# Kernel optimization log

Measured on AMD Instinct MI355X. Metric: run time of the kernel, lower is better.

The kernel has to match this reference:

```python
import jax, jax.numpy as jnp
import numpy as np

B, T, D, H = 2, 1024, 1024, 16
K = D            # key_dim = hidden * expand_k (1.0)
V = 2 * D        # value_dim = hidden * expand_v (2.0)
DK, DV = K // H, V // H
I = 2816         # SwiGLU intermediate
CONV = 4
EPS = 1e-6


def rmsnorm(x, w, eps=EPS):
    return x * jax.lax.rsqrt(jnp.mean(x * x, -1, keepdims=True) + eps) * w


def l2norm(x, eps=EPS):
    return x * jax.lax.rsqrt(jnp.sum(x * x, -1, keepdims=True) + eps)


def short_conv(x, w):
    # depthwise causal conv1d (kernel CONV, no bias) + silu; x [B,T,C], w [C,CONV]
    kern = w.T[:, None, :]  # [CONV, 1, C]
    y = jax.lax.conv_general_dilated(
        x, kern, (1,), [(CONV - 1, 0)],
        dimension_numbers=('NWC', 'WIO', 'NWC'),
        feature_group_count=x.shape[-1])
    return jax.nn.silu(y)


def setup_inputs() -> dict:
    key = jax.random.key(0)
    ks = jax.random.split(key, 20)
    p = lambda i, shape, s=0.02: jax.random.normal(ks[i], shape, jnp.float32) * s
    return dict(
        x=jax.random.normal(ks[0], (B, T, D), jnp.float32),
        norm1_w=jnp.ones((D,), jnp.float32),
        wq=p(1, (D, K)), wk=p(2, (D, K)), wv=p(3, (D, V)),
        conv_q=p(4, (K, CONV), 0.3), conv_k=p(5, (K, CONV), 0.3), conv_v=p(6, (V, CONV), 0.3),
        wb=p(7, (D, H)), wa=p(8, (D, H)),
        A_log=jnp.log(jax.random.uniform(ks[9], (H,), jnp.float32, 1.0, 16.0)),
        dt_bias=jnp.log(jnp.expm1(jax.random.uniform(ks[10], (H,), jnp.float32, 0.001, 0.1))),
        wg=p(11, (D, V)),
        o_norm_w=jnp.ones((DV,), jnp.float32),
        wo=p(12, (V, D)),
        norm2_w=jnp.ones((D,), jnp.float32),
        w1=p(13, (D, I)), w2=p(14, (I, D)), w3=p(15, (D, I)),
    )


def reference(x, norm1_w, wq, wk, wv, conv_q, conv_k, conv_v, wb, wa,
              A_log, dt_bias, wg, o_norm_w, wo, norm2_w, w1, w2, w3):
    h = rmsnorm(x, norm1_w)
    # projections + short causal conv (silu)
    q = short_conv(h @ wq, conv_q).reshape(B, T, H, DK)
    k = short_conv(h @ wk, conv_k).reshape(B, T, H, DK)
    v = short_conv(h @ wv, conv_v).reshape(B, T, H, DV)
    q = l2norm(q) * (DK ** -0.5)
    k = l2norm(k)
    beta = jax.nn.sigmoid(h @ wb)                              # [B,T,H]
    # mamba-style decay gate: g = -exp(A_log) * softplus(a + dt_bias)
    g = -jnp.exp(A_log) * jax.nn.softplus(h @ wa + dt_bias)   # [B,T,H]

    # gated delta rule: S_t = exp(g_t)*S_{t-1}; u_t = beta_t*(v_t - k_t^T S_t);
    # S_t += k_t u_t^T; o_t = q_t^T S_t
    def step(S, inp):
        qt, kt, vt, gt, bt = inp                               # [B,H,*]
        S = S * jnp.exp(gt)[..., None, None]
        u = (vt - jnp.einsum('bhk,bhkv->bhv', kt, S)) * bt[..., None]
        S = S + kt[..., None] * u[:, :, None, :]
        ot = jnp.einsum('bhk,bhkv->bhv', qt, S)
        return S, ot

    S0 = jnp.zeros((B, H, DK, DV), x.dtype)
    seq = (q.transpose(1, 0, 2, 3), k.transpose(1, 0, 2, 3),
           v.transpose(1, 0, 2, 3), g.transpose(1, 0, 2), beta.transpose(1, 0, 2))
    _, o = jax.lax.scan(step, S0, seq)
    o = o.transpose(1, 0, 2, 3)                                # [B,T,H,DV]

    # output gate: per-head RMSNorm * swish(gate), then out-projection
    gate = (h @ wg).reshape(B, T, H, DV)
    o = rmsnorm(o, o_norm_w) * gate * jax.nn.sigmoid(gate)
    x = x + o.reshape(B, T, V) @ wo

    # SwiGLU MLP with residual
    h2 = rmsnorm(x, norm2_w)
    return x + (jax.nn.silu(h2 @ w1) * (h2 @ w3)) @ w2
```

## Files before the change

### kernel.cpp

```cpp
#include <hip/hip_runtime.h>
#include <stdint.h>

typedef unsigned short u16;
typedef float f32x4 __attribute__((ext_vector_type(4)));
typedef __bf16 bf16x8 __attribute__((ext_vector_type(8)));
typedef unsigned short u16x8 __attribute__((ext_vector_type(8)));

#define N1P 6272

__device__ __forceinline__ u16 f2bf(float f) {
    union { float f; uint32_t u; } v; v.f = f;
    uint32_t u = v.u;
    return (u16)((u + 0x7FFFu + ((u >> 16) & 1u)) >> 16);
}
__device__ __forceinline__ float bf2f(u16 h) {
    union { uint32_t u; float f; } v; v.u = ((uint32_t)h) << 16; return v.f;
}
__device__ __forceinline__ float sigm(float x) { return 1.f / (1.f + __expf(-x)); }

__device__ __forceinline__ void async16(const u16* g, u16* l) {
    __builtin_amdgcn_global_load_lds((const __attribute__((address_space(1))) void*)g,
                                     (__attribute__((address_space(3))) void*)l, 16, 0, 0);
}

__device__ __forceinline__ int swz64(int row, int col) {
    return row * 128 + ((((col >> 3) ^ (row & 7)) << 3) + (col & 7)) * 2;
}
__device__ __forceinline__ bf16x8 frag64(const u16* m, int rowbase, int lane, int kk) {
    const int row = rowbase + (lane & 15);
    const int unit = (lane >> 4) + (kk << 2);
    return *(const bf16x8*)((const char*)m + row * 128 + ((unit ^ (row & 7)) << 4));
}

struct TJob { const float* src; u16* dst; int rows, cols, rowOff, rowStride, nOut, blkBase, gx, mode; };
struct TJobs { TJob j[10]; };

__global__ __launch_bounds__(256) void k_transpose_all(TJobs jobs, int njobs) {
    __shared__ float tile[32][33];
    const int bid = blockIdx.x;
    int ji = 0;
#pragma unroll
    for (int i = 1; i < 10; ++i)
        if (i < njobs && bid >= jobs.j[i].blkBase) ji = i;
    const TJob J = jobs.j[ji];
    const int bx = bid - J.blkBase;
    const int n0 = (bx % J.gx) * 32, k0 = (bx / J.gx) * 32;
    const int tx = threadIdx.x, ty = threadIdx.y;
#pragma unroll
    for (int j = 0; j < 32; j += 8) {
        int r = k0 + ty + j, c = n0 + tx;
        tile[ty + j][tx] = (r < J.rows && c < J.cols) ? J.src[(size_t)r * J.cols + c] : 0.f;
    }
    __syncthreads();
#pragma unroll
    for (int j = 0; j < 32; j += 8) {
        int n = n0 + ty + j, k = k0 + tx;
        if (n < J.nOut) {
            int drow = (J.mode == 0) ? (J.rowOff + n * J.rowStride)
                                     : (J.rowOff + ((n >> 4) << 5) + (n & 15));
            J.dst[(size_t)drow * J.rows + k] = f2bf(tile[tx][ty + j]);
        }
    }
}

__global__ __launch_bounds__(256) void k_rmsnorm(const float* __restrict__ x, const float* __restrict__ w,
                                                 u16* __restrict__ out) {
    const int row = blockIdx.x, tid = threadIdx.x, lane = tid & 63, wave = tid >> 6;
    const float4 v = ((const float4*)(x + (size_t)row * 1024))[tid];
    float ss = v.x * v.x + v.y * v.y + v.z * v.z + v.w * v.w;
#pragma unroll
    for (int o = 1; o < 64; o <<= 1) ss += __shfl_xor(ss, o);
    __shared__ float sred[4];
    if (lane == 0) sred[wave] = ss;
    __syncthreads();
    const float tot = sred[0] + sred[1] + sred[2] + sred[3];
    const float rn = rsqrtf(tot * (1.f / 1024.f) + 1e-6f);
    const float4 wv = ((const float4*)w)[tid];
    uint2 pk;
    pk.x = (uint32_t)f2bf(v.x * rn * wv.x) | ((uint32_t)f2bf(v.y * rn * wv.y) << 16);
    pk.y = (uint32_t)f2bf(v.z * rn * wv.z) | ((uint32_t)f2bf(v.w * rn * wv.w) << 16);
    *(uint2*)&out[(size_t)row * 1024 + tid * 4] = pk;
}

template <int TILE, int EPI>
__global__ __launch_bounds__(512) void k_gemm(const u16* __restrict__ A, const u16* __restrict__ Bt,
                                              void* __restrict__ Cout, const float* __restrict__ Res,
                                              int N, int Kd) {
    __shared__ __align__(16) char smem[TILE * 512];
    u16* Asb = (u16*)smem;
    u16* Bsb = (u16*)(smem + TILE * 256);
    constexpr int MB = 2048 / TILE;
    const int q = (int)gridDim.x >> 3;
    const int bid = blockIdx.x;
    const int wg = (bid & 7) * q + (bid >> 3);
    const int bm = wg & (MB - 1), bn = wg / MB;
    const int tid = threadIdx.x, lane = tid & 63, wave = tid >> 6;
    const int wm = wave >> 2, wn = wave & 3;
    constexpr int RS = TILE / 2, CS = TILE / 4;
    constexpr int FRM = RS / 16, FRN = CS / 16;
    constexpr int IS = TILE / 64;

    const int srow = wave * 8 + (lane >> 3);
    const int scol = ((lane & 7) ^ (lane >> 3)) * 8;
    const u16* gA = A + (size_t)(bm * TILE + srow) * Kd + scol;
    const u16* gB = Bt + (size_t)(bn * TILE + srow) * Kd + scol;

    f32x4 acc[FRM][FRN] = {};
    const int NT = Kd >> 6;

#pragma unroll
    for (int j = 0; j < IS; ++j) {
        async16(gA + (size_t)j * 64 * Kd, Asb + j * 4096 + wave * 512);
        async16(gB + (size_t)j * 64 * Kd, Bsb + j * 4096 + wave * 512);
    }
    asm volatile("s_waitcnt vmcnt(0)" ::: "memory");
    __syncthreads();

    int buf = 0;
    for (int t = 0; t < NT; ++t) {
        if (t + 1 < NT) {
            const int k0 = (t + 1) << 6;
            const int bo = (buf ^ 1) * TILE * 64;
#pragma unroll
            for (int j = 0; j < IS; ++j) {
                async16(gA + (size_t)j * 64 * Kd + k0, Asb + bo + j * 4096 + wave * 512);
                async16(gB + (size_t)j * 64 * Kd + k0, Bsb + bo + j * 4096 + wave * 512);
            }
        }
        const u16* Ab = Asb + buf * TILE * 64;
        const u16* Bb = Bsb + buf * TILE * 64;
#pragma unroll
        for (int kk = 0; kk < 2; ++kk) {
            bf16x8 af[FRM], bfr[FRN];
#pragma unroll
            for (int mi = 0; mi < FRM; ++mi) af[mi] = frag64(Ab, wm * RS + mi * 16, lane, kk);
#pragma unroll
            for (int ni = 0; ni < FRN; ++ni) bfr[ni] = frag64(Bb, wn * CS + ni * 16, lane, kk);
#pragma unroll
            for (int mi = 0; mi < FRM; ++mi)
#pragma unroll
                for (int ni = 0; ni < FRN; ++ni)
                    acc[mi][ni] = __builtin_amdgcn_mfma_f32_16x16x32_bf16(af[mi], bfr[ni], acc[mi][ni], 0, 0, 0);
        }
        asm volatile("s_waitcnt vmcnt(0)" ::: "memory");
        __syncthreads();
        buf ^= 1;
    }

    const int rsub = (lane >> 4) * 4;
    const int csub = lane & 15;

    if constexpr (EPI == 1) {
        float* ctile = (float*)smem;
#pragma unroll
        for (int mi = 0; mi < FRM; ++mi)
#pragma unroll
            for (int ni = 0; ni < FRN; ++ni)
#pragma unroll
                for (int r = 0; r < 4; ++r)
                    ctile[(wm * 32 + mi * 16 + rsub + r) * 68 + wn * 16 + ni * 16 + csub] = acc[mi][ni][r];
        __syncthreads();
#pragma unroll
        for (int k = 0; k < 2; ++k) {
            const int f = (tid + k * 512) * 4;
            const int r = f >> 6, c = f & 63;
            float4 v = *(const float4*)&ctile[r * 68 + c];
            const float4 rv = *(const float4*)&Res[(size_t)(bm * 64 + r) * N + bn * 64 + c];
            v.x += rv.x; v.y += rv.y; v.z += rv.z; v.w += rv.w;
            *(float4*)&((float*)Cout)[(size_t)(bm * 64 + r) * N + bn * 64 + c] = v;
        }
    } else if constexpr (EPI == 2) {
        u16* ctile = (u16*)smem;
#pragma unroll
        for (int mi = 0; mi < FRM; ++mi)
#pragma unroll
            for (int ni = 0; ni < FRN; ++ni)
#pragma unroll
                for (int r = 0; r < 4; ++r)
                    ctile[(wm * 64 + mi * 16 + rsub + r) * 132 + wn * 32 + ni * 16 + csub] =
                        f2bf(acc[mi][ni][r]);
        __syncthreads();
#pragma unroll
        for (int k = 0; k < 4; ++k) {
            const int f = (tid + k * 512) * 8;
            const int r = f >> 7, c = f & 127;
            *(u16x8*)&((u16*)Cout)[(size_t)(bm * 128 + r) * N + bn * 128 + c] =
                *(const u16x8*)&ctile[r * 132 + c];
        }
    } else {
        u16* ctile = (u16*)smem;
#pragma unroll
        for (int mi = 0; mi < FRM; ++mi)
#pragma unroll
            for (int r = 0; r < 4; ++r) {
                const float u1 = acc[mi][0][r];
                const float u3 = acc[mi][1][r];
                ctile[(wm * 64 + mi * 16 + rsub + r) * 68 + wn * 16 + csub] =
                    f2bf(u1 * sigm(u1) * u3);
            }
        __syncthreads();
#pragma unroll
        for (int k = 0; k < 2; ++k) {
            const int f = (tid + k * 512) * 8;
            const int r = f >> 6, c = f & 63;
            *(u16x8*)&((u16*)Cout)[(size_t)(bm * 128 + r) * N + bn * 64 + c] =
                *(const u16x8*)&ctile[r * 68 + c];
        }
    }
}

__global__ __launch_bounds__(256) void k_conv(const u16* __restrict__ P, const float* __restrict__ cwq,
                                              const float* __restrict__ cwk, const float* __restrict__ cwv,
                                              const float* __restrict__ A_log, const float* __restrict__ dtb,
                                              u16* __restrict__ Qb, u16* __restrict__ Kb,
                                              u16* __restrict__ Vb, float* __restrict__ Gl,
                                              float* __restrict__ Bbuf) {
    const int bid = blockIdx.x;
    const int row = (bid & 7) * 256 + (bid >> 3);
    const int t = row & 1023;
    const int tid = threadIdx.x;
    const long prow = (long)row * N1P;
#pragma unroll
    for (int p = 0; p < 2; ++p) {
        const int g = p * 256 + tid;
        const int c = g * 8;
        u16x8 taps[4];
#pragma unroll
        for (int j = 0; j < 4; ++j) {
            const int tt = t - 3 + j;
            if (tt >= 0) taps[j] = *(const u16x8*)&P[prow + (long)(j - 3) * N1P + c];
            else         taps[j] = u16x8{};
        }
        const float* cw = (c < 1024) ? (cwq + c * 4)
                          : (c < 2048) ? (cwk + (c - 1024) * 4)
                                       : (cwv + (c - 2048) * 4);
        float y[8];
#pragma unroll
        for (int e = 0; e < 8; ++e) {
            const float4 w = ((const float4*)cw)[e];
            float v = bf2f(taps[0][e]) * w.x + bf2f(taps[1][e]) * w.y +
                      bf2f(taps[2][e]) * w.z + bf2f(taps[3][e]) * w.w;
            y[e] = v * sigm(v);
        }
        if (c < 2048) {
            float ss = 0.f;
#pragma unroll
            for (int e = 0; e < 8; ++e) ss += y[e] * y[e];
            ss += __shfl_xor(ss, 1); ss += __shfl_xor(ss, 2); ss += __shfl_xor(ss, 4);
            const float rn = rsqrtf(ss + 1e-6f);
            const float sc = (c < 1024) ? rn * 0.125f : rn;
            u16x8 o;
#pragma unroll
            for (int e = 0; e < 8; ++e) o[e] = f2bf(y[e] * sc);
            if (c < 1024) *(u16x8*)&Qb[(size_t)row * 1024 + c] = o;
            else          *(u16x8*)&Kb[(size_t)row * 1024 + (c - 1024)] = o;
        } else {
            u16x8 o;
#pragma unroll
            for (int e = 0; e < 8; ++e) o[e] = f2bf(y[e]);
            *(u16x8*)&Vb[(size_t)row * 2048 + (c - 2048)] = o;
        }
    }
    if (tid < 32) {
        const int h = tid & 15;
        const float val = bf2f(P[prow + 4096 + tid]);
        if (tid < 16) {
            Bbuf[(size_t)row * 16 + h] = sigm(val);
        } else {
            const float a = val + dtb[h];
            const float sp = (a > 15.f) ? a : log1pf(__expf(a));
            Gl[(size_t)row * 16 + h] = -__expf(A_log[h]) * sp;
        }
    }
}

__global__ __launch_bounds__(256) void k_scan1(
    const u16* __restrict__ Qb, const u16* __restrict__ Kb, const u16* __restrict__ Vb,
    const float* __restrict__ Gl, const float* __restrict__ Bb,
    u16* __restrict__ CHW, u16* __restrict__ CHM, u16* __restrict__ CHQc,
    u16* __restrict__ CHKcT, u16* __restrict__ CHU0T, float* __restrict__ CHcC) {
    __shared__ __align__(16) char sm[66048];
    u16* Ql   = (u16*)(sm);
    u16* Kl   = (u16*)(sm + 8192);
    u16* VTb  = (u16*)(sm + 16384);
    u16* KT1b = (u16*)(sm + 32768);
    u16* Mim  = (u16*)(sm + 40960);
    u16* MTim = (u16*)(sm + 49152);
    u16* Tb   = (u16*)(sm + 57344);
    float* Tl    = (float*)sm;
    float* gcs   = (float*)(sm + 65536);
    float* betal = (float*)(sm + 65792);

    const int blk = blockIdx.x;
    const int bb = blk >> 8, h = (blk >> 4) & 15, ch = blk & 15;
    const int bhc = blk;
    const int tid = threadIdx.x, lane = tid & 63, wave = tid >> 6;
    const long rowbase = (long)bb * 1024 + ch * 64;

    if (tid < 64) {
        gcs[tid] = Gl[(rowbase + tid) * 16 + h];
        betal[tid] = Bb[(rowbase + tid) * 16 + h];
    }
    for (int u = tid; u < 512; u += 256) {
        int r = u >> 3, c8 = u & 7;
        uint4 kv = *(const uint4*)&Kb[(rowbase + r) * 1024 + h * 64 + c8 * 8];
        uint4 qv = *(const uint4*)&Qb[(rowbase + r) * 1024 + h * 64 + c8 * 8];
        int b = r * 128 + ((c8 ^ (r & 7)) << 4);
        *(uint4*)((char*)Kl + b) = kv;
        *(uint4*)((char*)Ql + b) = qv;
    }
    __syncthreads();
    if (wave == 0) {
        float g = gcs[lane];
#pragma unroll
        for (int off = 1; off < 64; off <<= 1) {
            float n = __shfl_up(g, off, 64);
            if (lane >= off) g += n;
        }
        gcs[lane] = g;
    }
    for (int u = tid; u < 1024; u += 256) {
        int r = u >> 4, c8 = u & 15;
        u16x8 vv = *(const u16x8*)&Vb[(rowbase + r) * 2048 + h * 128 + c8 * 8];
        float bsc = betal[r];
#pragma unroll
        for (int j = 0; j < 8; ++j) {
            int dv = c8 * 8 + j;
            *(u16*)((char*)VTb + swz64(dv, r)) = f2bf(bf2f(vv[j]) * bsc);
        }
    }
    f32x4 aQK[4] = {}, aKK[4] = {};
#pragma unroll
    for (int nt = 0; nt < 4; ++nt)
#pragma unroll
        for (int kk = 0; kk < 2; ++kk) {
            bf16x8 bq = frag64(Kl, nt * 16, lane, kk);
            aQK[nt] = __builtin_amdgcn_mfma_f32_16x16x32_bf16(frag64(Ql, wave * 16, lane, kk), bq, aQK[nt], 0, 0, 0);
            aKK[nt] = __builtin_amdgcn_mfma_f32_16x16x32_bf16(frag64(Kl, wave * 16, lane, kk), bq, aKK[nt], 0, 0, 0);
        }
    __syncthreads();

    const float gcsC = gcs[63];
    float am[4][4];
#pragma unroll
    for (int nt = 0; nt < 4; ++nt)
#pragma unroll
        for (int reg = 0; reg < 4; ++reg) {
            int t = wave * 16 + ((lane >> 4) << 2) + reg;
            int i = nt * 16 + (lane & 15);
            float dec = __expf(gcs[t] - gcs[i]);
            float mv = (i <= t) ? dec * aQK[nt][reg] : 0.f;
            *(u16*)((char*)CHM + (size_t)bhc * 8192 + swz64(t, i)) = f2bf(mv);
            float a = (i < t) ? betal[t] * dec * aKK[nt][reg] : 0.f;
            am[nt][reg] = -a;
            u16 amb = f2bf(-a);
            *(u16*)((char*)Mim + swz64(t, i)) = amb;
            *(u16*)((char*)MTim + swz64(i, t)) = amb;
        }
    for (int e = tid; e < 4096; e += 256) {
        int r = e >> 6, c = e & 63;
        int ib = swz64(r, c);
        float qv = bf2f(*(const u16*)((const char*)Ql + ib)) * __expf(gcs[r]);
        *(u16*)((char*)CHQc + (size_t)bhc * 8192 + ib) = f2bf(qv);
        float kv = bf2f(*(const u16*)((const char*)Kl + ib));
        int ob = swz64(c, r);
        *(u16*)((char*)KT1b + ob) = f2bf(kv * betal[r] * __expf(gcs[r]));
        *(u16*)((char*)CHKcT + (size_t)bhc * 8192 + ob) = f2bf(kv * __expf(gcsC - gcs[r]));
    }
    if (tid == 0) CHcC[bhc] = __expf(gcsC);
    __syncthreads();

#pragma unroll
    for (int nt = 0; nt < 4; ++nt)
#pragma unroll
        for (int reg = 0; reg < 4; ++reg) {
            int t = wave * 16 + ((lane >> 4) << 2) + reg;
            int i = nt * 16 + (lane & 15);
            float tv = (t == i) ? 1.f : am[nt][reg];
            Tl[t * 64 + i] = tv;
            *(u16*)((char*)Tb + swz64(t, i)) = f2bf(tv);
        }
    __syncthreads();

    const int hi = wave * 16 + 15;
#pragma unroll
    for (int j = 1; j <= 5; ++j) {
        f32x4 aM[4] = {};
#pragma unroll
        for (int nt = 0; nt < 4; ++nt) {
            if (nt * 16 > hi - (1 << j)) continue;
#pragma unroll
            for (int kk = 0; kk < 2; ++kk) {
                if (kk * 32 > hi) break;
                aM[nt] = __builtin_amdgcn_mfma_f32_16x16x32_bf16(
                    frag64(Mim, wave * 16, lane, kk), frag64(MTim, nt * 16, lane, kk), aM[nt], 0, 0, 0);
            }
        }
        __syncthreads();
#pragma unroll
        for (int nt = 0; nt < 4; ++nt)
#pragma unroll
            for (int reg = 0; reg < 4; ++reg) {
                int t = wave * 16 + ((lane >> 4) << 2) + reg;
                int i = nt * 16 + (lane & 15);
                float mv = (t - i >= (1 << j)) ? aM[nt][reg] : 0.f;
                u16 mb = f2bf(mv);
                *(u16*)((char*)Mim + swz64(t, i)) = mb;
                *(u16*)((char*)MTim + swz64(i, t)) = mb;
            }
        __syncthreads();
        f32x4 aT[4];
#pragma unroll
        for (int nt = 0; nt < 4; ++nt)
#pragma unroll
            for (int reg = 0; reg < 4; ++reg) {
                int t = wave * 16 + ((lane >> 4) << 2) + reg;
                int i = nt * 16 + (lane & 15);
                aT[nt][reg] = Tl[t * 64 + i];
            }
#pragma unroll
        for (int nt = 0; nt < 4; ++nt) {
            if (nt * 16 > hi - (1 << j)) continue;
#pragma unroll
            for (int kk = 0; kk < 2; ++kk) {
                if (kk * 32 > hi) break;
                aT[nt] = __builtin_amdgcn_mfma_f32_16x16x32_bf16(
                    frag64(Tb, wave * 16, lane, kk), frag64(MTim, nt * 16, lane, kk), aT[nt], 0, 0, 0);
            }
        }
#pragma unroll
        for (int nt = 0; nt < 4; ++nt)
#pragma unroll
            for (int reg = 0; reg < 4; ++reg) {
                int t = wave * 16 + ((lane >> 4) << 2) + reg;
                int i = nt * 16 + (lane & 15);
                Tl[t * 64 + i] = aT[nt][reg];
                *(u16*)((char*)Tb + swz64(t, i)) = f2bf(aT[nt][reg]);
            }
    }
    __syncthreads();

    {
        f32x4 aW[4] = {};
#pragma unroll
        for (int nt = 0; nt < 4; ++nt)
#pragma unroll
            for (int kk = 0; kk < 2; ++kk) {
                if (kk * 32 > hi) break;
                aW[nt] = __builtin_amdgcn_mfma_f32_16x16x32_bf16(
                    frag64(Tb, wave * 16, lane, kk), frag64(KT1b, nt * 16, lane, kk), aW[nt], 0, 0, 0);
            }
#pragma unroll
        for (int nt = 0; nt < 4; ++nt)
#pragma unroll
            for (int reg = 0; reg < 4; ++reg) {
                int r = wave * 16 + ((lane >> 4) << 2) + reg;
                int c = nt * 16 + (lane & 15);
                *(u16*)((char*)CHW + (size_t)bhc * 8192 + swz64(r, c)) = f2bf(aW[nt][reg]);
            }
    }
#pragma unroll
    for (int rt = 0; rt < 2; ++rt) {
        f32x4 aU[4] = {};
        int rb = (wave * 2 + rt) * 16;
#pragma unroll
        for (int nt = 0; nt < 4; ++nt)
#pragma unroll
            for (int kk = 0; kk < 2; ++kk) {
                if (kk * 32 > nt * 16 + 15) continue;
                aU[nt] = __builtin_amdgcn_mfma_f32_16x16x32_bf16(
                    frag64(VTb, rb, lane, kk), frag64(Tb, nt * 16, lane, kk), aU[nt], 0, 0, 0);
            }
#pragma unroll
        for (int nt = 0; nt < 4; ++nt)
#pragma unroll
            for (int reg = 0; reg < 4; ++reg) {
                int dv = rb + ((lane >> 4) << 2) + reg;
                int c = nt * 16 + (lane & 15);
                *(u16*)((char*)CHU0T + (size_t)bhc * 16384 + swz64(dv, c)) = f2bf(aU[nt][reg]);
            }
    }
}

__global__ __launch_bounds__(256) void k_scan2(
    const u16* __restrict__ CHW, const u16* __restrict__ CHM, const u16* __restrict__ CHQc,
    const u16* __restrict__ CHKcT, const u16* __restrict__ CHU0T, const float* __restrict__ CHcC,
    float* __restrict__ O) {
    __shared__ __align__(16) u16 stg[2][5 * 4096];
    __shared__ __align__(16) u16 STb[4096], uTl[4096];
    __shared__ float ST[64 * 66];
    const int blk = blockIdx.x;
    const int bb = blk >> 5, h = (blk >> 1) & 15, dvh = blk & 1;
    const int bh = bb * 16 + h;
    const int tid = threadIdx.x, lane = tid & 63, wave = tid >> 6;

    for (int e = tid; e < 64 * 66; e += 256) ST[e] = 0.f;
    for (int e = tid; e < 4096; e += 256) STb[e] = 0;

    auto stage = [&](int buf, int ch) {
        const size_t base = (size_t)(bh * 16 + ch);
        const u16* srcs[5] = { CHW + base * 4096, CHM + base * 4096, CHQc + base * 4096,
                               CHKcT + base * 4096, CHU0T + base * 8192 + dvh * 4096 };
#pragma unroll
        for (int s = 0; s < 5; ++s)
#pragma unroll
            for (int r = 0; r < 2; ++r) {
                int ub = r * 256 + wave * 64;
                async16(srcs[s] + (size_t)(ub + lane) * 8, &stg[buf][s * 4096 + ub * 8]);
            }
    };
    stage(0, 0);
    for (int ch = 0; ch < 16; ++ch) {
        const int cur = ch & 1;
        asm volatile("s_waitcnt vmcnt(0)" ::: "memory");
        __syncthreads();
        if (ch < 15) stage(cur ^ 1, ch + 1);
        const u16* sW = &stg[cur][0];
        const u16* sM = &stg[cur][4096];
        const u16* sQc = &stg[cur][8192];
        const u16* sKcT = &stg[cur][12288];
        const u16* sU0 = &stg[cur][16384];
        {
            f32x4 acc[4] = {};
#pragma unroll
            for (int nt = 0; nt < 4; ++nt)
#pragma unroll
                for (int kk = 0; kk < 2; ++kk)
                    acc[nt] = __builtin_amdgcn_mfma_f32_16x16x32_bf16(
                        frag64(STb, wave * 16, lane, kk), frag64(sW, nt * 16, lane, kk), acc[nt], 0, 0, 0);
#pragma unroll
            for (int nt = 0; nt < 4; ++nt)
#pragma unroll
                for (int reg = 0; reg < 4; ++reg) {
                    int dv = wave * 16 + ((lane >> 4) << 2) + reg;
                    int c = nt * 16 + (lane & 15);
                    int b = swz64(dv, c);
                    float u0 = bf2f(*(const u16*)((const char*)sU0 + b));
                    *(u16*)((char*)uTl + b) = f2bf(u0 - acc[nt][reg]);
                }
        }
        __syncthreads();
        f32x4 accO[4] = {}, accS[4] = {};
#pragma unroll
        for (int nt = 0; nt < 4; ++nt)
#pragma unroll
            for (int kk = 0; kk < 2; ++kk) {
                accO[nt] = __builtin_amdgcn_mfma_f32_16x16x32_bf16(
                    frag64(sM, wave * 16, lane, kk), frag64(uTl, nt * 16, lane, kk), accO[nt], 0, 0, 0);
                accO[nt] = __builtin_amdgcn_mfma_f32_16x16x32_bf16(
                    frag64(sQc, wave * 16, lane, kk), frag64(STb, nt * 16, lane, kk), accO[nt], 0, 0, 0);
                accS[nt] = __builtin_amdgcn_mfma_f32_16x16x32_bf16(
                    frag64(uTl, wave * 16, lane, kk), frag64(sKcT, nt * 16, lane, kk), accS[nt], 0, 0, 0);
            }
        __syncthreads();
        const float cC = CHcC[bh * 16 + ch];
#pragma unroll
        for (int nt = 0; nt < 4; ++nt)
#pragma unroll
            for (int reg = 0; reg < 4; ++reg) {
                int rr = wave * 16 + ((lane >> 4) << 2) + reg;
                int cc = nt * 16 + (lane & 15);
                O[((size_t)(bb * 1024 + ch * 64 + rr)) * 2048 + h * 128 + dvh * 64 + cc] = accO[nt][reg];
                float ns = cC * ST[rr * 66 + cc] + accS[nt][reg];
                ST[rr * 66 + cc] = ns;
                *(u16*)((char*)STb + swz64(rr, cc)) = f2bf(ns);
            }
    }
}

__global__ __launch_bounds__(256) void k_gate(const float* __restrict__ O, const u16* __restrict__ P,
                                              const float* __restrict__ onw, u16* __restrict__ OG) {
    const int row = blockIdx.x;
    const int tid = threadIdx.x, lane = tid & 63, wave = tid >> 6;
#pragma unroll
    for (int p = 0; p < 4; ++p) {
        const int h = p * 4 + wave;
        const int dv = lane * 2;
        const float2 o2 = *(const float2*)&O[(size_t)row * 2048 + h * 128 + dv];
        float ss = o2.x * o2.x + o2.y * o2.y;
#pragma unroll
        for (int o = 1; o < 64; o <<= 1) ss += __shfl_xor(ss, o);
        const float rn = rsqrtf(ss * (1.f / 128.f) + 1e-6f);
        const float g0 = bf2f(P[(size_t)row * N1P + 4128 + h * 128 + dv]);
        const float g1 = bf2f(P[(size_t)row * N1P + 4128 + h * 128 + dv + 1]);
        const float r0 = o2.x * rn * onw[dv] * g0 * sigm(g0);
        const float r1 = o2.y * rn * onw[dv + 1] * g1 * sigm(g1);
        const uint32_t pk = (uint32_t)f2bf(r0) | ((uint32_t)f2bf(r1) << 16);
        *(uint32_t*)&OG[(size_t)row * 2048 + h * 128 + dv] = pk;
    }
}

extern "C" void kernel_launch(void* const* d_in, const int* in_sizes, int n_in,
                              void* d_out, int out_size, void* d_ws, size_t ws_size,
                              hipStream_t stream) {
    const float* x   = (const float*)d_in[0];
    const float* n1w = (const float*)d_in[1];
    const float* wq  = (const float*)d_in[2];
    const float* wk  = (const float*)d_in[3];
    const float* wv  = (const float*)d_in[4];
    const float* cq  = (const float*)d_in[5];
    const float* ck  = (const float*)d_in[6];
    const float* cv  = (const float*)d_in[7];
    const float* wb  = (const float*)d_in[8];
    const float* wa  = (const float*)d_in[9];
    const float* Alg = (const float*)d_in[10];
    const float* dtb = (const float*)d_in[11];
    const float* wg  = (const float*)d_in[12];
    const float* onw = (const float*)d_in[13];
    const float* wo  = (const float*)d_in[14];
    const float* n2w = (const float*)d_in[15];
    const float* w1  = (const float*)d_in[16];
    const float* w2  = (const float*)d_in[17];
    const float* w3  = (const float*)d_in[18];

    if (ws_size < 114819072ULL) return;

    char* ws = (char*)d_ws;
    u16*   WcatT = (u16*)(ws + 0);
    u16*   WoT   = (u16*)(ws + 12845056);
    u16*   W13T  = (u16*)(ws + 17039360);
    u16*   W2T   = (u16*)(ws + 28573696);
    u16*   hA    = (u16*)(ws + 34340864);
    u16*   P     = (u16*)(ws + 38535168);
    u16*   Qb    = (u16*)(ws + 64225280);
    u16*   Kb    = (u16*)(ws + 68419584);
    u16*   Vb    = (u16*)(ws + 72613888);
    float* Gl    = (float*)(ws + 81002496);
    float* Bbf   = (float*)(ws + 81133568);
    float* O     = (float*)(ws + 81264640);
    u16*   CHKcT = (u16*)(ws + 98041856);
    u16*   CHU0T = (u16*)(ws + 102236160);
    float* CHcC  = (float*)(ws + 110624768);
    u16*   CHW   = WcatT;
    u16*   CHM   = (u16*)(ws + 4194304);
    u16*   CHQc  = (u16*)(ws + 8388608);
    u16*   Mm  = Qb;
    u16*   OG  = Vb;
    float* X2  = O;
    u16*   h2A = hA;

    TJobs tj;
    tj.j[0] = { wq, WcatT, 1024, 1024,    0, 1, 1024,     0, 32, 0 };
    tj.j[1] = { wk, WcatT, 1024, 1024, 1024, 1, 1024,  1024, 32, 0 };
    tj.j[2] = { wv, WcatT, 1024, 2048, 2048, 1, 2048,  2048, 64, 0 };
    tj.j[3] = { wb, WcatT, 1024,   16, 4096, 1,   16,  4096,  1, 0 };
    tj.j[4] = { wa, WcatT, 1024,   16, 4112, 1,   16,  4128,  1, 0 };
    tj.j[5] = { wg, WcatT, 1024, 2048, 4128, 1, 2144,  4160, 67, 0 };
    tj.j[6] = { wo, WoT,   2048, 1024,    0, 1, 1024,  6304, 32, 0 };
    tj.j[7] = { w1, W13T,  1024, 2816,    0, 1, 2816,  8352, 88, 1 };
    tj.j[8] = { w3, W13T,  1024, 2816,   16, 1, 2816, 11168, 88, 1 };
    tj.j[9] = { w2, W2T,   2816, 1024,    0, 1, 1024, 13984, 32, 0 };
    k_transpose_all<<<16800, dim3(32, 8), 0, stream>>>(tj, 10);

    k_rmsnorm<<<2048, 256, 0, stream>>>(x, n1w, hA);
    k_gemm<128, 2><<<784, 512, 0, stream>>>(hA, WcatT, P, nullptr, N1P, 1024);

    k_conv<<<2048, 256, 0, stream>>>(P, cq, ck, cv, Alg, dtb, Qb, Kb, Vb, Gl, Bbf);

    k_scan1<<<512, 256, 0, stream>>>(Qb, Kb, Vb, Gl, Bbf, CHW, CHM, CHQc, CHKcT, CHU0T, CHcC);
    k_scan2<<<64, 256, 0, stream>>>(CHW, CHM, CHQc, CHKcT, CHU0T, CHcC, O);

    k_gate<<<2048, 256, 0, stream>>>(O, P, onw, OG);
    k_gemm<64, 1><<<512, 512, 0, stream>>>(OG, WoT, X2, x, 1024, 2048);

    k_rmsnorm<<<2048, 256, 0, stream>>>(X2, n2w, h2A);
    k_gemm<128, 3><<<704, 512, 0, stream>>>(h2A, W13T, Mm, nullptr, 2816, 1024);
    k_gemm<64, 1><<<512, 512, 0, stream>>>(Mm, W2T, (float*)d_out, X2, 1024, 2816);
}
```

Measured before the change: 247.5 us.

## Add 256x256-tile pipelined GEMM for input projection and SwiGLU up-projection

Adds a new GEMM kernel with 256x256 output tiles, 128 KB of LDS, a two-stage software pipeline that interleaves async global-to-LDS loads with MFMA phases, and s_setprio around the MFMA blocks. It replaces the 128-tile GEMM for the fused QKV/gate projection and for the W1/W3 SwiGLU GEMM. The fused projection width is padded to 6400 so it divides by 256, and workspace offsets and transpose jobs are shifted to match. Larger tiles raise arithmetic intensity and cut global traffic, but give fewer blocks (200 and 176) on a 256-CU device, which risks underfilling the GPU and adds padded work.

```diff
diff --git a/kernel.cpp b/kernel.cpp
--- a/kernel.cpp
+++ b/kernel.cpp
@@ -6,7 +6,7 @@
 typedef __bf16 bf16x8 __attribute__((ext_vector_type(8)));
 typedef unsigned short u16x8 __attribute__((ext_vector_type(8)));
 
-#define N1P 6272
+#define N1P 6400
 
 __device__ __forceinline__ u16 f2bf(float f) {
     union { float f; uint32_t u; } v; v.f = f;
@@ -80,6 +80,137 @@
     pk.x = (uint32_t)f2bf(v.x * rn * wv.x) | ((uint32_t)f2bf(v.y * rn * wv.y) << 16);
     pk.y = (uint32_t)f2bf(v.z * rn * wv.z) | ((uint32_t)f2bf(v.w * rn * wv.w) << 16);
     *(uint2*)&out[(size_t)row * 1024 + tid * 4] = pk;
+}
+
+template <int EPI>
+__global__ __launch_bounds__(512, 2) void k_gemm256(const u16* __restrict__ A, const u16* __restrict__ Bt,
+                                                    u16* __restrict__ Cout, int N, int Kd) {
+    __shared__ __align__(16) u16 L[65536];
+    const int q8 = (int)gridDim.x >> 3;
+    const int bid = blockIdx.x;
+    const int wg = (bid & 7) * q8 + (bid >> 3);
+    const int bm = wg & 7, bn = wg >> 3;
+    const int tid = threadIdx.x, lane = tid & 63, wave = tid >> 6;
+    const int wm = wave >> 2, wn = wave & 3;
+
+    const int scol = ((tid & 7) ^ ((tid >> 3) & 7)) * 8;
+    const u16* gA = A + (size_t)(bm * 256 + (tid >> 3)) * Kd + scol;
+    const u16* gB = Bt + (size_t)(bn * 256 + (tid >> 3)) * Kd + scol;
+    u16* dstT = L + tid * 8;
+
+    const int NT = Kd >> 6;
+    const int NI = NT >> 1;
+
+    auto issue = [&](const u16* g, int mtx, int kt, int h) {
+        u16* d = dstT + (kt & 1) * 32768 + mtx * 16384 + h * 8192;
+        const u16* s = g + (size_t)(h * 128) * Kd + kt * 64;
+        async16(s, d);
+        async16(s + (size_t)64 * Kd, d + 4096);
+    };
+
+    issue(gB, 1, 0, 0); issue(gB, 1, 0, 1);
+    issue(gA, 0, 0, 0); issue(gA, 0, 0, 1);
+    issue(gB, 1, 1, 0); issue(gB, 1, 1, 1);
+    asm volatile("s_waitcnt vmcnt(4)" ::: "memory");
+    __builtin_amdgcn_s_barrier();
+
+    f32x4 acc[8][4] = {};
+    bf16x8 bq[4][2];
+
+    for (int i = 0; i < NI; ++i) {
+        const int kt0 = 2 * i;
+#pragma unroll
+        for (int p = 0; p < 8; ++p) {
+            const int half = p >> 2;
+            const int q = p & 3;
+            const u16* Ab = L + half * 32768;
+            const u16* Bb = L + half * 32768 + 16384;
+            if (q == 0) {
+#pragma unroll
+                for (int ni = 0; ni < 4; ++ni)
+#pragma unroll
+                    for (int kk = 0; kk < 2; ++kk)
+                        bq[ni][kk] = frag64(Bb, wn * 64 + ni * 16, lane, kk);
+            }
+            bf16x8 af[2][2];
+#pragma unroll
+            for (int j = 0; j < 2; ++j)
+#pragma unroll
+                for (int kk = 0; kk < 2; ++kk)
+                    af[j][kk] = frag64(Ab, wm * 128 + (2 * q + j) * 16, lane, kk);
+            if (p == 0) { if (kt0 + 1 < NT) issue(gA, 0, kt0 + 1, 0); }
+            if (p == 1) { if (kt0 + 1 < NT) issue(gA, 0, kt0 + 1, 1);
+                          if (kt0 + 2 < NT) issue(gB, 1, kt0 + 2, 0); }
+            if (p == 2) { if (kt0 + 2 < NT) issue(gB, 1, kt0 + 2, 1); }
+            if (p == 4) { if (kt0 + 2 < NT) issue(gA, 0, kt0 + 2, 0); }
+            if (p == 5) { if (kt0 + 2 < NT) issue(gA, 0, kt0 + 2, 1);
+                          if (kt0 + 3 < NT) issue(gB, 1, kt0 + 3, 0); }
+            if (p == 6) { if (kt0 + 3 < NT) issue(gB, 1, kt0 + 3, 1); }
+            if (p == 3) { if (i + 1 < NI) { asm volatile("s_waitcnt vmcnt(4)" ::: "memory"); }
+                          else            { asm volatile("s_waitcnt vmcnt(0)" ::: "memory"); } }
+            if (p == 7) { if (i + 1 < NI) { asm volatile("s_waitcnt vmcnt(4)" ::: "memory"); } }
+            __builtin_amdgcn_s_barrier();
+            __builtin_amdgcn_s_setprio(1);
+#pragma unroll
+            for (int j = 0; j < 2; ++j)
+#pragma unroll
+                for (int ni = 0; ni < 4; ++ni)
+#pragma unroll
+                    for (int kk = 0; kk < 2; ++kk)
+                        acc[2 * q + j][ni] = __builtin_amdgcn_mfma_f32_16x16x32_bf16(
+                            af[j][kk], bq[ni][kk], acc[2 * q + j][ni], 0, 0, 0);
+            __builtin_amdgcn_s_setprio(0);
+            __builtin_amdgcn_s_barrier();
+        }
+    }
+
+    const int rsub = (lane >> 4) * 4, csub = lane & 15;
+    if constexpr (EPI == 2) {
+        u16* ct = L;
+#pragma unroll
+        for (int r = 0; r < 2; ++r) {
+            if (wm == r) {
+#pragma unroll
+                for (int mi = 0; mi < 8; ++mi)
+#pragma unroll
+                    for (int ni = 0; ni < 4; ++ni)
+#pragma unroll
+                        for (int rr = 0; rr < 4; ++rr)
+                            ct[(mi * 16 + rsub + rr) * 264 + wn * 64 + ni * 16 + csub] =
+                                f2bf(acc[mi][ni][rr]);
+            }
+            __syncthreads();
+#pragma unroll
+            for (int k = 0; k < 8; ++k) {
+                const int f = (tid + k * 512) * 8;
+                const int r2 = f >> 8, c = f & 255;
+                *(u16x8*)&Cout[(size_t)(bm * 256 + r * 128 + r2) * N + bn * 256 + c] =
+                    *(const u16x8*)&ct[r2 * 264 + c];
+            }
+            __syncthreads();
+        }
+    } else {
+        u16* ct = L;
+#pragma unroll
+        for (int mi = 0; mi < 8; ++mi)
+#pragma unroll
+            for (int g = 0; g < 2; ++g)
+#pragma unroll
+                for (int rr = 0; rr < 4; ++rr) {
+                    const float u1 = acc[mi][2 * g][rr];
+                    const float u3 = acc[mi][2 * g + 1][rr];
+                    ct[(wm * 128 + mi * 16 + rsub + rr) * 132 + wn * 32 + g * 16 + csub] =
+                        f2bf(u1 * sigm(u1) * u3);
+                }
+        __syncthreads();
+#pragma unroll
+        for (int k = 0; k < 8; ++k) {
+            const int f = (tid + k * 512) * 8;
+            const int r2 = f >> 7, c = f & 127;
+            *(u16x8*)&Cout[(size_t)(bm * 256 + r2) * N + bn * 128 + c] =
+                *(const u16x8*)&ct[r2 * 132 + c];
+        }
+    }
 }
 
 template <int TILE, int EPI>
@@ -149,63 +280,23 @@
 
     const int rsub = (lane >> 4) * 4;
     const int csub = lane & 15;
-
-    if constexpr (EPI == 1) {
-        float* ctile = (float*)smem;
-#pragma unroll
-        for (int mi = 0; mi < FRM; ++mi)
-#pragma unroll
-            for (int ni = 0; ni < FRN; ++ni)
-#pragma unroll
-                for (int r = 0; r < 4; ++r)
-                    ctile[(wm * 32 + mi * 16 + rsub + r) * 68 + wn * 16 + ni * 16 + csub] = acc[mi][ni][r];
-        __syncthreads();
-#pragma unroll
-        for (int k = 0; k < 2; ++k) {
-            const int f = (tid + k * 512) * 4;
-            const int r = f >> 6, c = f & 63;
-            float4 v = *(const float4*)&ctile[r * 68 + c];
-            const float4 rv = *(const float4*)&Res[(size_t)(bm * 64 + r) * N + bn * 64 + c];
-            v.x += rv.x; v.y += rv.y; v.z += rv.z; v.w += rv.w;
-            *(float4*)&((float*)Cout)[(size_t)(bm * 64 + r) * N + bn * 64 + c] = v;
-        }
-    } else if constexpr (EPI == 2) {
-        u16* ctile = (u16*)smem;
-#pragma unroll
-        for (int mi = 0; mi < FRM; ++mi)
-#pragma unroll
-            for (int ni = 0; ni < FRN; ++ni)
-#pragma unroll
-                for (int r = 0; r < 4; ++r)
-                    ctile[(wm * 64 + mi * 16 + rsub + r) * 132 + wn * 32 + ni * 16 + csub] =
-                        f2bf(acc[mi][ni][r]);
-        __syncthreads();
-#pragma unroll
-        for (int k = 0; k < 4; ++k) {
-            const int f = (tid + k * 512) * 8;
-            const int r = f >> 7, c = f & 127;
-            *(u16x8*)&((u16*)Cout)[(size_t)(bm * 128 + r) * N + bn * 128 + c] =
-                *(const u16x8*)&ctile[r * 132 + c];
-        }
-    } else {
-        u16* ctile = (u16*)smem;
-#pragma unroll
-        for (int mi = 0; mi < FRM; ++mi)
-#pragma unroll
-            for (int r = 0; r < 4; ++r) {
-                const float u1 = acc[mi][0][r];
-                const float u3 = acc[mi][1][r];
-                ctile[(wm * 64 + mi * 16 + rsub + r) * 68 + wn * 16 + csub] =
-                    f2bf(u1 * sigm(u1) * u3);
-            }
-        __syncthreads();
-#pragma unroll
-        for (int k = 0; k < 2; ++k) {
-            const int f = (tid + k * 512) * 8;
-            const int r = f >> 6, c = f & 63;
-            *(u16x8*)&((u16*)Cout)[(size_t)(bm * 128 + r) * N + bn * 64 + c] =
-                *(const u16x8*)&ctile[r * 68 + c];
-        }
+    float* ctile = (float*)smem;
+#pragma unroll
+    for (int mi = 0; mi < FRM; ++mi)
+#pragma unroll
+        for (int ni = 0; ni < FRN; ++ni)
+#pragma unroll
+            for (int r = 0; r < 4; ++r)
+                ctile[(wm * 32 + mi * 16 + rsub + r) * 68 + wn * 16 + ni * 16 + csub] = acc[mi][ni][r];
+    __syncthreads();
+#pragma unroll
+    for (int k = 0; k < 2; ++k) {
+        const int f = (tid + k * 512) * 4;
+        const int r = f >> 6, c = f & 63;
+        float4 v = *(const float4*)&ctile[r * 68 + c];
+        const float4 rv = *(const float4*)&Res[(size_t)(bm * 64 + r) * N + bn * 64 + c];
+        v.x += rv.x; v.y += rv.y; v.z += rv.z; v.w += rv.w;
+        *(float4*)&((float*)Cout)[(size_t)(bm * 64 + r) * N + bn * 64 + c] = v;
     }
 }
 
@@ -613,24 +704,24 @@
     const float* w2  = (const float*)d_in[17];
     const float* w3  = (const float*)d_in[18];
 
-    if (ws_size < 114819072ULL) return;
+    if (ws_size < 111413248ULL) return;
 
     char* ws = (char*)d_ws;
     u16*   WcatT = (u16*)(ws + 0);
-    u16*   WoT   = (u16*)(ws + 12845056);
-    u16*   W13T  = (u16*)(ws + 17039360);
-    u16*   W2T   = (u16*)(ws + 28573696);
-    u16*   hA    = (u16*)(ws + 34340864);
-    u16*   P     = (u16*)(ws + 38535168);
-    u16*   Qb    = (u16*)(ws + 64225280);
-    u16*   Kb    = (u16*)(ws + 68419584);
-    u16*   Vb    = (u16*)(ws + 72613888);
-    float* Gl    = (float*)(ws + 81002496);
-    float* Bbf   = (float*)(ws + 81133568);
-    float* O     = (float*)(ws + 81264640);
-    u16*   CHKcT = (u16*)(ws + 98041856);
-    u16*   CHU0T = (u16*)(ws + 102236160);
-    float* CHcC  = (float*)(ws + 110624768);
+    u16*   WoT   = (u16*)(ws + 13107200);
+    u16*   W13T  = (u16*)(ws + 17301504);
+    u16*   W2T   = (u16*)(ws + 28835840);
+    u16*   hA    = (u16*)(ws + 34603008);
+    u16*   P     = (u16*)(ws + 38797312);
+    u16*   Qb    = (u16*)(ws + 65011712);
+    u16*   Kb    = (u16*)(ws + 69206016);
+    u16*   Vb    = (u16*)(ws + 73400320);
+    float* Gl    = (float*)(ws + 81788928);
+    float* Bbf   = (float*)(ws + 81920000);
+    float* O     = (float*)(ws + 82051072);
+    u16*   CHKcT = (u16*)(ws + 98828288);
+    u16*   CHU0T = (u16*)(ws + 103022592);
+    float* CHcC  = (float*)(ws + 111411200);
     u16*   CHW   = WcatT;
     u16*   CHM   = (u16*)(ws + 4194304);
     u16*   CHQc  = (u16*)(ws + 8388608);
@@ -645,15 +736,15 @@
     tj.j[2] = { wv, WcatT, 1024, 2048, 2048, 1, 2048,  2048, 64, 0 };
     tj.j[3] = { wb, WcatT, 1024,   16, 4096, 1,   16,  4096,  1, 0 };
     tj.j[4] = { wa, WcatT, 1024,   16, 4112, 1,   16,  4128,  1, 0 };
-    tj.j[5] = { wg, WcatT, 1024, 2048, 4128, 1, 2144,  4160, 67, 0 };
-    tj.j[6] = { wo, WoT,   2048, 1024,    0, 1, 1024,  6304, 32, 0 };
-    tj.j[7] = { w1, W13T,  1024, 2816,    0, 1, 2816,  8352, 88, 1 };
-    tj.j[8] = { w3, W13T,  1024, 2816,   16, 1, 2816, 11168, 88, 1 };
-    tj.j[9] = { w2, W2T,   2816, 1024,    0, 1, 1024, 13984, 32, 0 };
-    k_transpose_all<<<16800, dim3(32, 8), 0, stream>>>(tj, 10);
+    tj.j[5] = { wg, WcatT, 1024, 2048, 4128, 1, 2272,  4160, 71, 0 };
+    tj.j[6] = { wo, WoT,   2048, 1024,    0, 1, 1024,  6432, 32, 0 };
+    tj.j[7] = { w1, W13T,  1024, 2816,    0, 1, 2816,  8480, 88, 1 };
+    tj.j[8] = { w3, W13T,  1024, 2816,   16, 1, 2816, 11296, 88, 1 };
+    tj.j[9] = { w2, W2T,   2816, 1024,    0, 1, 1024, 14112, 32, 0 };
+    k_transpose_all<<<16928, dim3(32, 8), 0, stream>>>(tj, 10);
 
     k_rmsnorm<<<2048, 256, 0, stream>>>(x, n1w, hA);
-    k_gemm<128, 2><<<784, 512, 0, stream>>>(hA, WcatT, P, nullptr, N1P, 1024);
+    k_gemm256<2><<<200, 512, 0, stream>>>(hA, WcatT, P, N1P, 1024);
 
     k_conv<<<2048, 256, 0, stream>>>(P, cq, ck, cv, Alg, dtb, Qb, Kb, Vb, Gl, Bbf);
 
@@ -664,6 +755,6 @@
     k_gemm<64, 1><<<512, 512, 0, stream>>>(OG, WoT, X2, x, 1024, 2048);
 
     k_rmsnorm<<<2048, 256, 0, stream>>>(X2, n2w, h2A);
-    k_gemm<128, 3><<<704, 512, 0, stream>>>(h2A, W13T, Mm, nullptr, 2816, 1024);
+    k_gemm256<3><<<176, 512, 0, stream>>>(h2A, W13T, Mm, 2816, 1024);
     k_gemm<64, 1><<<512, 512, 0, stream>>>(Mm, W2T, (float*)d_out, X2, 1024, 2816);
 }
```

Result: faster. 242.3 us (-2.1%).
